# Optimization experiments

Measured on AMD Instinct MI355X. Metric: run time of the kernel, lower is better.

The kernel has to match this reference:

```python
import jax, jax.numpy as jnp
import numpy as np

B, S, D_IN, D_OUT, H = 4, 2048, 1024, 1024, 16
HD = D_OUT // H


def setup_inputs() -> dict:
    key = jax.random.key(0)
    ks = jax.random.split(key, 6)
    s_in = 1.0 / np.sqrt(D_IN)
    s_out = 1.0 / np.sqrt(D_OUT)
    return {
        "x": jax.random.normal(ks[0], (B, S, D_IN), dtype=jnp.float32),
        "Wq": jax.random.uniform(ks[1], (D_IN, D_OUT), jnp.float32, -s_in, s_in),
        "Wk": jax.random.uniform(ks[2], (D_IN, D_OUT), jnp.float32, -s_in, s_in),
        "Wv": jax.random.uniform(ks[3], (D_IN, D_OUT), jnp.float32, -s_in, s_in),
        "Wo": jax.random.uniform(ks[4], (D_OUT, D_OUT), jnp.float32, -s_out, s_out),
        "bo": jax.random.uniform(ks[5], (D_OUT,), jnp.float32, -s_out, s_out),
    }


def reference(x, Wq, Wk, Wv, Wo, bo):
    b, s, _ = x.shape
    # project and split heads: (b, h, s, hd)
    def heads(w):
        return (x @ w).reshape(b, s, H, HD).transpose(0, 2, 1, 3)
    q, k, v = heads(Wq), heads(Wk), heads(Wv)
    scores = jnp.einsum("bhqd,bhkd->bhqk", q, k) / np.sqrt(HD).astype(np.float32)
    causal = jnp.tril(jnp.ones((s, s), dtype=bool))  # True = keep
    scores = jnp.where(causal, scores, -jnp.inf)
    attn = jax.nn.softmax(scores, axis=-1)
    ctx = jnp.einsum("bhqk,bhkd->bhqd", attn, v)
    ctx = ctx.transpose(0, 2, 1, 3).reshape(b, s, D_OUT)
    return ctx @ Wo.T + bo
```

## Files before the change

### kernel.cpp

```cpp
#include <hip/hip_runtime.h>
#include <hip/hip_bf16.h>

#define BB   4
#define SS   2048
#define DIN  1024
#define DOUT 1024
#define NH   16
#define HDIM 64

typedef __hip_bfloat16 bf16;
typedef __attribute__((ext_vector_type(8))) short short8;
typedef __attribute__((ext_vector_type(4))) float floatx4;

#define AS1(p) ((const __attribute__((address_space(1))) void*)(p))
#define AS3(p) ((__attribute__((address_space(3))) void*)(p))

__global__ void prep_all_kernel(const float* __restrict__ x,
                                const float* __restrict__ Wq, const float* __restrict__ Wk,
                                const float* __restrict__ Wv, const float* __restrict__ Wo,
                                bf16* __restrict__ xb, bf16* __restrict__ wt,
                                bf16* __restrict__ wob) {
    __shared__ float tile[64][65];
    const int bid = blockIdx.x;
    const int tid = threadIdx.x;
    if (bid < 4096 || bid >= 4864) {
        const float* src = (bid < 4096) ? x : Wo;
        bf16* dst        = (bid < 4096) ? xb : wob;
        const int  rb    = (bid < 4096) ? bid : (bid - 4864);
        size_t i = ((size_t)rb * 256 + tid) * 8;
        float4 a = *(const float4*)(src + i);
        float4 b = *(const float4*)(src + i + 4);
        bf16 o[8] __attribute__((aligned(16)));
        o[0] = __float2bfloat16(a.x); o[1] = __float2bfloat16(a.y);
        o[2] = __float2bfloat16(a.z); o[3] = __float2bfloat16(a.w);
        o[4] = __float2bfloat16(b.x); o[5] = __float2bfloat16(b.y);
        o[6] = __float2bfloat16(b.z); o[7] = __float2bfloat16(b.w);
        *(short8*)(dst + i) = *(short8*)o;
        return;
    }
    const int pb = bid - 4096;
    const int kt = pb & 15;
    const int nt = pb >> 4;
    const int k0 = kt * 64, n0 = nt * 64;
    const float* W = (n0 < 1024) ? Wq : (n0 < 2048 ? Wk : Wv);
    const int col0 = n0 & 1023;
    {
        const int kl = tid >> 2, nc = (tid & 3) * 16;
        const float* src = W + (size_t)(k0 + kl) * 1024 + col0 + nc;
        #pragma unroll
        for (int i = 0; i < 16; i += 4) {
            float4 v = *(const float4*)(src + i);
            tile[kl][nc + i + 0] = v.x; tile[kl][nc + i + 1] = v.y;
            tile[kl][nc + i + 2] = v.z; tile[kl][nc + i + 3] = v.w;
        }
    }
    __syncthreads();
    {
        const int nl = tid >> 2, kc = (tid & 3) * 16;
        bf16 o[16] __attribute__((aligned(16)));
        #pragma unroll
        for (int i = 0; i < 16; ++i) o[i] = __float2bfloat16(tile[kc + i][nl]);
        bf16* dst = wt + (size_t)(n0 + nl) * 1024 + k0 + kc;
        *(short8*)dst       = *(short8*)&o[0];
        *(short8*)(dst + 8) = *(short8*)&o[8];
    }
}

template<int EPI>
__global__ __launch_bounds__(256) void gemm_bt_kernel(
    const bf16* __restrict__ A, const bf16* __restrict__ Bt,
    void* __restrict__ C, const float* __restrict__ bias, int K, int ldc,
    bf16* __restrict__ vt) {
    __shared__ __align__(16) bf16 As[128][32];
    __shared__ __align__(16) bf16 Bs[128][32];
    const int tid  = threadIdx.x;
    const int wave = tid >> 6, lane = tid & 63;
    const int lm   = lane & 15, quad = lane >> 4;
    const int wm   = (wave >> 1) * 64, wn = (wave & 1) * 64;
    const size_t rowA0 = (size_t)blockIdx.x * 128;
    const size_t rowB0 = (size_t)blockIdx.y * 128;
    const int srow = wave * 16 + (lane >> 2);
    const int skc  = (lane & 3) * 8;

    floatx4 acc[4][4] = {};

    for (int k0 = 0; k0 < K; k0 += 32) {
        __syncthreads();
        #pragma unroll
        for (int r = 0; r < 2; ++r) {
            const bf16* gA = A  + (rowA0 + r * 64 + srow) * (size_t)K + k0 + skc;
            __builtin_amdgcn_global_load_lds(AS1(gA), AS3(&As[r * 64 + wave * 16][0]), 16, 0, 0);
            const bf16* gB = Bt + (rowB0 + r * 64 + srow) * (size_t)K + k0 + skc;
            __builtin_amdgcn_global_load_lds(AS1(gB), AS3(&Bs[r * 64 + wave * 16][0]), 16, 0, 0);
        }
        __syncthreads();
        short8 a[4], b[4];
        #pragma unroll
        for (int i = 0; i < 4; ++i) a[i] = *(const short8*)&As[wm + i * 16 + lm][quad * 8];
        #pragma unroll
        for (int j = 0; j < 4; ++j) b[j] = *(const short8*)&Bs[wn + j * 16 + lm][quad * 8];
        #pragma unroll
        for (int i = 0; i < 4; ++i)
            #pragma unroll
            for (int j = 0; j < 4; ++j)
                acc[i][j] = __builtin_amdgcn_mfma_f32_16x16x32_bf16(a[i], b[j], acc[i][j], 0, 0, 0);
    }

    if (EPI == 0 && rowB0 >= 2048) {
        #pragma unroll
        for (int i = 0; i < 4; ++i) {
            size_t row = rowA0 + wm + i * 16 + quad * 4;
            const size_t b = row >> 11;
            const int    s = (int)(row & 2047);
            #pragma unroll
            for (int j = 0; j < 4; ++j) {
                const int col = (int)(rowB0 - 2048) + wn + j * 16 + lm;
                bf16 o[4] __attribute__((aligned(8)));
                #pragma unroll
                for (int r = 0; r < 4; ++r) o[r] = __float2bfloat16(acc[i][j][r]);
                *(uint64_t*)(vt + ((b * 16 + (col >> 6)) * 64 + (col & 63)) * (size_t)SS + s)
                    = *(uint64_t*)o;
            }
        }
        return;
    }

    #pragma unroll
    for (int i = 0; i < 4; ++i) {
        size_t row = rowA0 + wm + i * 16 + quad * 4;
        #pragma unroll
        for (int j = 0; j < 4; ++j) {
            size_t col = rowB0 + wn + j * 16 + lm;
            float bv = (EPI == 1) ? bias[col] : 0.0f;
            #pragma unroll
            for (int r = 0; r < 4; ++r) {
                if (EPI == 0)
                    ((bf16*)C)[(row + r) * ldc + col] = __float2bfloat16(acc[i][j][r]);
                else
                    ((float*)C)[(row + r) * ldc + col] = acc[i][j][r] + bv;
            }
        }
    }
}

#define PSTR 68
__global__ __launch_bounds__(256, 3) void flash_attn_kernel(
    const bf16* __restrict__ qkv, const bf16* __restrict__ vt, bf16* __restrict__ ctx) {
    __shared__ __align__(16) bf16 Ks[2][64 * 64];
    __shared__ __align__(16) bf16 Vs[2][64 * 64];
    __shared__ __align__(16) bf16 Pl[4][32 * PSTR + 8];
    const int tid  = threadIdx.x;
    const int wave = tid >> 6, lane = tid & 63;
    const int lm   = lane & 15, quad = lane >> 4;

    const int id  = blockIdx.x;
    const int jl  = (id >> 3) & 7;
    const int bh  = (id & 7) * 8 + jl;
    const int p   = 15 - (id >> 6);
    const int b = bh >> 4, h = bh & 15;

    const int lane8r = lane >> 3;
    const int schunk = (lane & 7) ^ lane8r;

    const bf16* kg = qkv + (size_t)b * SS * 3072 + 1024 + h * 64 + schunk * 8;
    const bf16* vg = vt + (size_t)(b * NH + h) * 64 * SS + schunk * 8;

    bf16* Pw = &Pl[wave][0];

    const int qb = p * 128 + wave * 32;
    const int nkt = 2 * p + 2;

    short8 bq[2][2];
    #pragma unroll
    for (int g = 0; g < 2; ++g) {
        const bf16* qp = qkv + ((size_t)(b * SS + qb + g * 16 + lm)) * 3072 + h * 64 + quad * 8;
        bq[g][0] = *(const short8*)qp;
        bq[g][1] = *(const short8*)(qp + 32);
    }

    floatx4 o[2][4] = {};
    float lsum[2] = {0.f, 0.f};

    #pragma unroll
    for (int c = 0; c < 2; ++c) {
        const int row = c * 32 + wave * 8 + lane8r;
        __builtin_amdgcn_global_load_lds(AS1(kg + (size_t)row * 3072), AS3(&Ks[0][(c * 256 + wave * 64) * 8]), 16, 0, 0);
        __builtin_amdgcn_global_load_lds(AS1(vg + (size_t)row * SS), AS3(&Vs[0][(c * 256 + wave * 64) * 8]), 16, 0, 0);
    }

    #pragma unroll 1
    for (int kt = 0; kt < nkt; ++kt) {
        const int cur = kt & 1;
        __syncthreads();
        if (kt + 1 < nkt) {
            #pragma unroll
            for (int c = 0; c < 2; ++c) {
                const int row = c * 32 + wave * 8 + lane8r;
                __builtin_amdgcn_global_load_lds(AS1(kg + (size_t)((kt + 1) * 64 + row) * 3072),
                                                 AS3(&Ks[cur ^ 1][(c * 256 + wave * 64) * 8]), 16, 0, 0);
                __builtin_amdgcn_global_load_lds(AS1(vg + (size_t)row * SS + (kt + 1) * 64),
                                                 AS3(&Vs[cur ^ 1][(c * 256 + wave * 64) * 8]), 16, 0, 0);
            }
        }

        const int sw = lm & 7;
        const bf16* Ksb = &Ks[cur][0];
        const bf16* Vsb = &Vs[cur][0];
        short8 ka[4][2], va[4][2];
        #pragma unroll
        for (int nt = 0; nt < 4; ++nt) {
            const int r0 = (nt * 16 + lm) * 64;
            ka[nt][0] = *(const short8*)(Ksb + r0 + ((quad ^ sw) * 8));
            ka[nt][1] = *(const short8*)(Ksb + r0 + (((4 + quad) ^ sw) * 8));
            va[nt][0] = *(const short8*)(Vsb + r0 + ((quad ^ sw) * 8));
            va[nt][1] = *(const short8*)(Vsb + r0 + (((4 + quad) ^ sw) * 8));
        }

        #pragma unroll
        for (int g = 0; g < 2; ++g) {
            floatx4 sc[4];
            #pragma unroll
            for (int nt = 0; nt < 4; ++nt) {
                floatx4 z = {};
                z = __builtin_amdgcn_mfma_f32_16x16x32_bf16(ka[nt][0], bq[g][0], z, 0, 0, 0);
                z = __builtin_amdgcn_mfma_f32_16x16x32_bf16(ka[nt][1], bq[g][1], z, 0, 0, 0);
                sc[nt] = z;
            }
            if (kt * 64 + 63 > qb + g * 16) {
                const int qrow = qb + g * 16 + lm;
                #pragma unroll
                for (int nt = 0; nt < 4; ++nt)
                    #pragma unroll
                    for (int r = 0; r < 4; ++r)
                        if (kt * 64 + nt * 16 + quad * 4 + r > qrow) sc[nt][r] = -1e30f;
            }
            #pragma unroll
            for (int nt = 0; nt < 4; ++nt) {
                bf16 pk[4] __attribute__((aligned(8)));
                #pragma unroll
                for (int r = 0; r < 4; ++r) {
                    float pv = __builtin_amdgcn_exp2f(sc[nt][r] * 0.18033688f);
                    lsum[g] += pv;
                    pk[r] = __float2bfloat16(pv);
                }
                *(uint64_t*)&Pw[(g * 16 + lm) * PSTR + nt * 16 + quad * 4] = *(uint64_t*)pk;
            }
        }
        #pragma unroll
        for (int g = 0; g < 2; ++g) {
            const short8 ap0 = *(const short8*)&Pw[(g * 16 + lm) * PSTR + quad * 8];
            const short8 ap1 = *(const short8*)&Pw[(g * 16 + lm) * PSTR + 32 + quad * 8];
            #pragma unroll
            for (int t = 0; t < 4; ++t) {
                o[g][t] = __builtin_amdgcn_mfma_f32_16x16x32_bf16(ap0, va[t][0], o[g][t], 0, 0, 0);
                o[g][t] = __builtin_amdgcn_mfma_f32_16x16x32_bf16(ap1, va[t][1], o[g][t], 0, 0, 0);
            }
        }
    }

    #pragma unroll
    for (int g = 0; g < 2; ++g) {
        float rsum = lsum[g];
        rsum += __shfl_xor(rsum, 16);
        rsum += __shfl_xor(rsum, 32);
        float rl[4];
        #pragma unroll
        for (int r = 0; r < 4; ++r) rl[r] = 1.0f / __shfl(rsum, quad * 4 + r);
        #pragma unroll
        for (int t = 0; t < 4; ++t)
            #pragma unroll
            for (int r = 0; r < 4; ++r) {
                size_t row = (size_t)b * SS + qb + g * 16 + quad * 4 + r;
                ctx[row * 1024 + h * 64 + t * 16 + lm] = __float2bfloat16(o[g][t][r] * rl[r]);
            }
    }
}

extern "C" void kernel_launch(void* const* d_in, const int* in_sizes, int n_in,
                              void* d_out, int out_size, void* d_ws, size_t ws_size,
                              hipStream_t stream) {
    const float* x  = (const float*)d_in[0];
    const float* Wq = (const float*)d_in[1];
    const float* Wk = (const float*)d_in[2];
    const float* Wv = (const float*)d_in[3];
    const float* Wo = (const float*)d_in[4];
    const float* bo = (const float*)d_in[5];

    char* ws = (char*)d_ws;
    bf16* xb  = (bf16*)ws;  ws += (size_t)8192 * 1024 * 2;
    bf16* wt  = (bf16*)ws;  ws += (size_t)3072 * 1024 * 2;
    bf16* wob = (bf16*)ws;  ws += (size_t)1024 * 1024 * 2;
    bf16* qkv = (bf16*)ws;  ws += (size_t)8192 * 3072 * 2;
    bf16* vtb = (bf16*)ws;  ws += (size_t)BB * NH * HDIM * SS * 2;
    bf16* ctx = xb;

    prep_all_kernel<<<5376, 256, 0, stream>>>(x, Wq, Wk, Wv, Wo, xb, wt, wob);
    gemm_bt_kernel<0><<<dim3(64, 24), 256, 0, stream>>>(xb, wt, (void*)qkv, nullptr, 1024, 3072, vtb);
    flash_attn_kernel<<<1024, 256, 0, stream>>>(qkv, vtb, ctx);
    gemm_bt_kernel<1><<<dim3(64, 8), 256, 0, stream>>>(ctx, wob, d_out, bo, 1024, 1024, nullptr);
}
```

Baseline: 262.6 us.

## Double GEMM K-tile to 64 and XOR-swizzle LDS layout

The projection GEMM kernel now stages 64-wide K tiles instead of 32, which halves the number of barrier-separated load iterations. It also applies an XOR swizzle to the 16-byte chunk placement in LDS, both on the global-to-LDS load and on the fragment reads, to avoid bank conflicts. LDS use doubles to 32KB per block, which may reduce occupancy.

```diff
diff --git a/kernel.cpp b/kernel.cpp
--- a/kernel.cpp
+++ b/kernel.cpp
@@ -71,39 +71,52 @@
     const bf16* __restrict__ A, const bf16* __restrict__ Bt,
     void* __restrict__ C, const float* __restrict__ bias, int K, int ldc,
     bf16* __restrict__ vt) {
-    __shared__ __align__(16) bf16 As[128][32];
-    __shared__ __align__(16) bf16 Bs[128][32];
+    __shared__ __align__(16) bf16 As[128][64];
+    __shared__ __align__(16) bf16 Bs[128][64];
     const int tid  = threadIdx.x;
     const int wave = tid >> 6, lane = tid & 63;
     const int lm   = lane & 15, quad = lane >> 4;
     const int wm   = (wave >> 1) * 64, wn = (wave & 1) * 64;
     const size_t rowA0 = (size_t)blockIdx.x * 128;
     const size_t rowB0 = (size_t)blockIdx.y * 128;
-    const int srow = wave * 16 + (lane >> 2);
-    const int skc  = (lane & 3) * 8;
+
+    const int srow8  = lane >> 3;
+    const int schunk = (lane & 7) ^ srow8;
+    const int sw     = lm & 7;
 
     floatx4 acc[4][4] = {};
 
-    for (int k0 = 0; k0 < K; k0 += 32) {
+    for (int k0 = 0; k0 < K; k0 += 64) {
         __syncthreads();
         #pragma unroll
-        for (int r = 0; r < 2; ++r) {
-            const bf16* gA = A  + (rowA0 + r * 64 + srow) * (size_t)K + k0 + skc;
-            __builtin_amdgcn_global_load_lds(AS1(gA), AS3(&As[r * 64 + wave * 16][0]), 16, 0, 0);
-            const bf16* gB = Bt + (rowB0 + r * 64 + srow) * (size_t)K + k0 + skc;
-            __builtin_amdgcn_global_load_lds(AS1(gB), AS3(&Bs[r * 64 + wave * 16][0]), 16, 0, 0);
+        for (int j = 0; j < 4; ++j) {
+            const int rbase = (wave * 4 + j) * 8;
+            const bf16* gA = A  + (rowA0 + rbase + srow8) * (size_t)K + k0 + schunk * 8;
+            __builtin_amdgcn_global_load_lds(AS1(gA), AS3(&As[rbase][0]), 16, 0, 0);
+            const bf16* gB = Bt + (rowB0 + rbase + srow8) * (size_t)K + k0 + schunk * 8;
+            __builtin_amdgcn_global_load_lds(AS1(gB), AS3(&Bs[rbase][0]), 16, 0, 0);
         }
         __syncthreads();
-        short8 a[4], b[4];
-        #pragma unroll
-        for (int i = 0; i < 4; ++i) a[i] = *(const short8*)&As[wm + i * 16 + lm][quad * 8];
-        #pragma unroll
-        for (int j = 0; j < 4; ++j) b[j] = *(const short8*)&Bs[wn + j * 16 + lm][quad * 8];
+        short8 a[4][2], b[4][2];
+        #pragma unroll
+        for (int i = 0; i < 4; ++i) {
+            const int r = wm + i * 16 + lm;
+            a[i][0] = *(const short8*)&As[r][((quad    ) ^ sw) * 8];
+            a[i][1] = *(const short8*)&As[r][((quad + 4) ^ sw) * 8];
+        }
+        #pragma unroll
+        for (int j = 0; j < 4; ++j) {
+            const int r = wn + j * 16 + lm;
+            b[j][0] = *(const short8*)&Bs[r][((quad    ) ^ sw) * 8];
+            b[j][1] = *(const short8*)&Bs[r][((quad + 4) ^ sw) * 8];
+        }
         #pragma unroll
         for (int i = 0; i < 4; ++i)
             #pragma unroll
-            for (int j = 0; j < 4; ++j)
-                acc[i][j] = __builtin_amdgcn_mfma_f32_16x16x32_bf16(a[i], b[j], acc[i][j], 0, 0, 0);
+            for (int j = 0; j < 4; ++j) {
+                acc[i][j] = __builtin_amdgcn_mfma_f32_16x16x32_bf16(a[i][0], b[j][0], acc[i][j], 0, 0, 0);
+                acc[i][j] = __builtin_amdgcn_mfma_f32_16x16x32_bf16(a[i][1], b[j][1], acc[i][j], 0, 0, 0);
+            }
     }
 
     if (EPI == 0 && rowB0 >= 2048) {
```

Measured after the change: 252.0 us. 1.04x faster.
